# Performance work log

Hardware: AMD Instinct MI355X
Metric: run time of the kernel (lower is better)

## Reference

```python
import jax, jax.numpy as jnp
import numpy as np

T, C, H, W, D = 100, 2, 128, 128, 8192


def setup_inputs() -> dict:
    key = jax.random.key(0)
    k1, k2, k3, k4 = jax.random.split(key, 4)
    # event histogram: nonnegative intensities per (time, polarity, y, x)
    hist = jax.random.uniform(k1, (T, C, H, W), dtype=jnp.float32)
    # torchhd Random(vsa='MAP') tables are random bipolar {-1,+1} vectors
    time_w = jnp.sign(jax.random.normal(k2, (T, D), dtype=jnp.float32))
    pol_w = jnp.sign(jax.random.normal(k3, (C, D), dtype=jnp.float32))
    pos_w = jnp.sign(jax.random.normal(k4, (H * W, D), dtype=jnp.float32))
    return {"hist": hist, "time_w": time_w, "pol_w": pol_w, "pos_w": pos_w}


def reference(hist, time_w, pol_w, pos_w):
    # Original: for every nonzero pixel, bind (elementwise mul in MAP)
    # pos_hv * pol_hv * time_hv, scale by intensity, accumulate, then sign.
    # Equivalent fused form:
    #   out_d = sign( sum_{t,p,n} hist[t,p,n] * pos_w[n,d] * pol_w[p,d] * time_w[t,d] )
    t, c, h, w = hist.shape
    flat = hist.reshape(t, c, h * w)                      # [T, 2, H*W]
    # intensity-weighted sum of position HVs per (t, p): one GEMM over H*W
    acc = jnp.einsum('tpn,nd->tpd', flat, pos_w)          # [T, 2, D]
    # bind with polarity and time HVs, reduce over t and p
    gesture = jnp.einsum('tpd,pd,td->d', acc, pol_w, time_w)  # [D]
    return jnp.sign(gesture)
```

## Files before the change

### kernel.cpp

```cpp
#include <hip/hip_runtime.h>
#include <cstdint>
#include <cstddef>

#define MROWS 200
#define PM    224
#define KDIM  16384
#define DDIM  8192
#define KSL   16
#define KPER  (KDIM / KSL)
#define BK    32

typedef __bf16 bf16x8 __attribute__((ext_vector_type(8)));
typedef float  f32x4  __attribute__((ext_vector_type(4)));

static __device__ __forceinline__ unsigned short f2bf_rne(float f) {
    unsigned int u = __float_as_uint(f);
    unsigned int r = (u + 0x7FFFu + ((u >> 16) & 1u)) >> 16;
    return (unsigned short)r;
}
static __device__ __forceinline__ float bf2f(unsigned short s) {
    return __uint_as_float(((unsigned int)s) << 16);
}

static __device__ __forceinline__ void gld_lds16(const unsigned short* g,
                                                 unsigned short* l) {
    __builtin_amdgcn_global_load_lds(
        (const __attribute__((address_space(1))) unsigned int*)g,
        (__attribute__((address_space(3))) unsigned int*)l, 16, 0, 0);
}

__global__ __launch_bounds__(256) void zero_kernel(float* __restrict__ out) {
    out[blockIdx.x * 256 + threadIdx.x] = 0.f;
}

__global__ __launch_bounds__(256) void prep_kernel(const float* __restrict__ hist,
                                                   unsigned short* __restrict__ ahi,
                                                   unsigned short* __restrict__ alo) {
    const int g  = blockIdx.x * 256 + threadIdx.x;
    const int m  = g >> 11;
    const int gc = g & 2047;
    const int f  = (m >> 1) & 3;
    const int sgc = (gc & ~3) | ((gc & 3) ^ f);
    alignas(16) unsigned short hi[8], lo[8];
    if (m < MROWS) {
        const float* src = hist + (size_t)m * KDIM + sgc * 8;
        float4 a = *(const float4*)(src);
        float4 b = *(const float4*)(src + 4);
        const float v[8] = {a.x, a.y, a.z, a.w, b.x, b.y, b.z, b.w};
#pragma unroll
        for (int i = 0; i < 8; ++i) {
            unsigned short h = f2bf_rne(v[i]);
            hi[i] = h;
            lo[i] = f2bf_rne(v[i] - bf2f(h));
        }
    } else {
#pragma unroll
        for (int i = 0; i < 8; ++i) { hi[i] = 0; lo[i] = 0; }
    }
    *(uint4*)(ahi + (size_t)g * 8) = *(const uint4*)hi;
    *(uint4*)(alo + (size_t)g * 8) = *(const uint4*)lo;
}

__global__ __launch_bounds__(256, 2)
void gemm_kernel(const unsigned short* __restrict__ ahi,
                 const unsigned short* __restrict__ alo,
                 const float* __restrict__ pos,
                 const float* __restrict__ time_w,
                 const float* __restrict__ pol_w,
                 float* __restrict__ out) {
    __shared__ alignas(16) unsigned short As0[PM * BK];
    __shared__ alignas(16) unsigned short As1[PM * BK];
    __shared__ alignas(16) unsigned short Bs[128][40];
    __shared__ float sPart[128];

    const int t     = threadIdx.x;
    const int ks    = blockIdx.x;
    const int n0    = blockIdx.y * 128;
    const int kbase = ks * KPER;

    const int lane = t & 63;
    const int wv   = t >> 6;
    const int wm   = (wv & 1) * 112;
    const int wn   = (wv >> 1) * 64;
    const int l15  = lane & 15;
    const int q8   = (lane >> 4) * 8;
    const int qg   = (lane >> 4) ^ ((l15 >> 1) & 3);

    if (t < 128) sPart[t] = 0.f;

    const int lr = lane >> 2, lg = lane & 3;
    const unsigned short* gA[7];
    unsigned short* lA[7];
#pragma unroll
    for (int i = 0; i < 7; ++i) {
        const int cc = wv * 7 + i;
        const int pl = (cc >= 14) ? 1 : 0;
        const int ch = cc - pl * 14;
        gA[i] = (pl ? alo : ahi) + (size_t)(ch * 16 + lr) * KDIM + kbase + lg * 8;
        lA[i] = (pl ? As1 : As0) + ch * 512;
    }

    const int bk2 = (t & 15) * 2;
    const int bnb = (t >> 4) * 8;
    const float* gB0 = pos + ((size_t)kbase + bk2) * DDIM + n0 + bnb;
    const float* gB1 = gB0 + DDIM;

    f32x4 acc[7][4];
#pragma unroll
    for (int s = 0; s < 7; ++s)
#pragma unroll
        for (int j = 0; j < 4; ++j) acc[s][j] = (f32x4){0.f, 0.f, 0.f, 0.f};

    for (int kk = 0; kk < KPER; kk += BK) {
        const float* b0 = gB0 + (size_t)kk * DDIM;
        const float* b1 = gB1 + (size_t)kk * DDIM;
        float4 x0 = *(const float4*)(b0);
        float4 x1 = *(const float4*)(b0 + 4);
        float4 y0 = *(const float4*)(b1);
        float4 y1 = *(const float4*)(b1 + 4);

        __syncthreads();

#pragma unroll
        for (int i = 0; i < 7; ++i) gld_lds16(gA[i] + kk, lA[i]);

        {
            const float xv[8] = {x0.x, x0.y, x0.z, x0.w, x1.x, x1.y, x1.z, x1.w};
            const float yv[8] = {y0.x, y0.y, y0.z, y0.w, y1.x, y1.y, y1.z, y1.w};
#pragma unroll
            for (int j = 0; j < 8; ++j) {
                unsigned int w = (__float_as_uint(xv[j]) >> 16) |
                                 (__float_as_uint(yv[j]) & 0xFFFF0000u);
                *(unsigned int*)&Bs[bnb + j][bk2] = w;
            }
        }

        __syncthreads();

        uint4 fb[4];
#pragma unroll
        for (int j = 0; j < 4; ++j)
            fb[j] = *(const uint4*)&Bs[wn + j * 16 + l15][q8];

#pragma unroll
        for (int s = 0; s < 7; ++s) {
            const int mr = wm + s * 16 + l15;
            const uint4 fa0 = *(const uint4*)&As0[mr * 32 + qg * 8];
            const uint4 fa1 = *(const uint4*)&As1[mr * 32 + qg * 8];
#pragma unroll
            for (int j = 0; j < 4; ++j) {
                acc[s][j] = __builtin_amdgcn_mfma_f32_16x16x32_bf16(
                    __builtin_bit_cast(bf16x8, fa0),
                    __builtin_bit_cast(bf16x8, fb[j]), acc[s][j], 0, 0, 0);
                acc[s][j] = __builtin_amdgcn_mfma_f32_16x16x32_bf16(
                    __builtin_bit_cast(bf16x8, fa1),
                    __builtin_bit_cast(bf16x8, fb[j]), acc[s][j], 0, 0, 0);
            }
        }
    }

    const int qrow = (lane >> 4) * 4;
#pragma unroll
    for (int j = 0; j < 4; ++j) {
        const int col = wn + j * 16 + l15;
        const int d   = n0 + col;
        const float p0 = pol_w[d];
        const float p1 = pol_w[DDIM + d];
        float part = 0.f;
#pragma unroll
        for (int s = 0; s < 7; ++s)
#pragma unroll
            for (int r = 0; r < 4; ++r) {
                const int m = wm + s * 16 + qrow + r;
                if (m < MROWS) {
                    const float w = time_w[(size_t)(m >> 1) * DDIM + d] *
                                    ((m & 1) ? p1 : p0);
                    part += w * acc[s][j][r];
                }
            }
        atomicAdd(&sPart[col], part);
    }
    __syncthreads();
    if (t < 128) atomicAdd(out + n0 + t, sPart[t]);
}

__global__ __launch_bounds__(256) void sign_kernel(float* __restrict__ out) {
    int d = blockIdx.x * 256 + threadIdx.x;
    float s = out[d];
    out[d] = (s > 0.f) ? 1.f : ((s < 0.f) ? -1.f : 0.f);
}

extern "C" void kernel_launch(void* const* d_in, const int* in_sizes, int n_in,
                              void* d_out, int out_size, void* d_ws, size_t ws_size,
                              hipStream_t stream) {
    const float* hist   = (const float*)d_in[0];
    const float* time_w = (const float*)d_in[1];
    const float* pol_w  = (const float*)d_in[2];
    const float* pos_w  = (const float*)d_in[3];
    float* out = (float*)d_out;

    unsigned short* ahi = (unsigned short*)d_ws;
    unsigned short* alo = ahi + (size_t)PM * KDIM;
    (void)in_sizes; (void)n_in; (void)out_size; (void)ws_size;

    zero_kernel<<<DDIM / 256, 256, 0, stream>>>(out);
    prep_kernel<<<(PM * (KDIM / 8)) / 256, 256, 0, stream>>>(hist, ahi, alo);
    gemm_kernel<<<dim3(KSL, DDIM / 128), 256, 0, stream>>>(ahi, alo, pos_w,
                                                           time_w, pol_w, out);
    sign_kernel<<<DDIM / 256, 256, 0, stream>>>(out);
}
```

Measured before the change: 752.1 us.

## Software-pipeline GEMM with double-buffered A tiles and B register prefetch

Restructures the K loop of the GEMM so that A tiles are double-buffered in LDS and B rows are prefetched two steps ahead into registers. Explicit waitcnt, s_barrier and sched_barrier calls order the memory ops, and setprio raises wave priority during the MFMA section. The goal is to overlap global loads with MFMA work instead of stalling on each tile. In exchange it uses more LDS, which may limit occupancy, and more registers. Wrap-around indexing issues redundant loads at the end of the loop, and the hand-tuned vmcnt count makes correctness depend on load ordering.

```diff
diff --git a/kernel.cpp b/kernel.cpp
--- a/kernel.cpp
+++ b/kernel.cpp
@@ -9,6 +9,7 @@
 #define KSL   16
 #define KPER  (KDIM / KSL)
 #define BK    32
+#define NSTEP (KPER / BK)
 
 typedef __bf16 bf16x8 __attribute__((ext_vector_type(8)));
 typedef float  f32x4  __attribute__((ext_vector_type(4)));
@@ -68,8 +69,7 @@
                  const float* __restrict__ time_w,
                  const float* __restrict__ pol_w,
                  float* __restrict__ out) {
-    __shared__ alignas(16) unsigned short As0[PM * BK];
-    __shared__ alignas(16) unsigned short As1[PM * BK];
+    __shared__ alignas(16) unsigned short As[2][2][PM * BK];
     __shared__ alignas(16) unsigned short Bs[128][40];
     __shared__ float sPart[128];
 
@@ -90,14 +90,15 @@
 
     const int lr = lane >> 2, lg = lane & 3;
     const unsigned short* gA[7];
-    unsigned short* lA[7];
+    unsigned short* lA[2][7];
 #pragma unroll
     for (int i = 0; i < 7; ++i) {
         const int cc = wv * 7 + i;
         const int pl = (cc >= 14) ? 1 : 0;
         const int ch = cc - pl * 14;
         gA[i] = (pl ? alo : ahi) + (size_t)(ch * 16 + lr) * KDIM + kbase + lg * 8;
-        lA[i] = (pl ? As1 : As0) + ch * 512;
+        lA[0][i] = &As[0][pl][ch * 512];
+        lA[1][i] = &As[1][pl][ch * 512];
     }
 
     const int bk2 = (t & 15) * 2;
@@ -111,51 +112,88 @@
 #pragma unroll
         for (int j = 0; j < 4; ++j) acc[s][j] = (f32x4){0.f, 0.f, 0.f, 0.f};
 
-    for (int kk = 0; kk < KPER; kk += BK) {
-        const float* b0 = gB0 + (size_t)kk * DDIM;
-        const float* b1 = gB1 + (size_t)kk * DDIM;
-        float4 x0 = *(const float4*)(b0);
-        float4 x1 = *(const float4*)(b0 + 4);
-        float4 y0 = *(const float4*)(b1);
-        float4 y1 = *(const float4*)(b1 + 4);
-
-        __syncthreads();
-
-#pragma unroll
-        for (int i = 0; i < 7; ++i) gld_lds16(gA[i] + kk, lA[i]);
-
-        {
-            const float xv[8] = {x0.x, x0.y, x0.z, x0.w, x1.x, x1.y, x1.z, x1.w};
-            const float yv[8] = {y0.x, y0.y, y0.z, y0.w, y1.x, y1.y, y1.z, y1.w};
-#pragma unroll
-            for (int j = 0; j < 8; ++j) {
-                unsigned int w = (__float_as_uint(xv[j]) >> 16) |
-                                 (__float_as_uint(yv[j]) & 0xFFFF0000u);
-                *(unsigned int*)&Bs[bnb + j][bk2] = w;
-            }
-        }
-
-        __syncthreads();
-
-        uint4 fb[4];
-#pragma unroll
-        for (int j = 0; j < 4; ++j)
-            fb[j] = *(const uint4*)&Bs[wn + j * 16 + l15][q8];
-
-#pragma unroll
-        for (int s = 0; s < 7; ++s) {
-            const int mr = wm + s * 16 + l15;
-            const uint4 fa0 = *(const uint4*)&As0[mr * 32 + qg * 8];
-            const uint4 fa1 = *(const uint4*)&As1[mr * 32 + qg * 8];
-#pragma unroll
-            for (int j = 0; j < 4; ++j) {
-                acc[s][j] = __builtin_amdgcn_mfma_f32_16x16x32_bf16(
-                    __builtin_bit_cast(bf16x8, fa0),
-                    __builtin_bit_cast(bf16x8, fb[j]), acc[s][j], 0, 0, 0);
-                acc[s][j] = __builtin_amdgcn_mfma_f32_16x16x32_bf16(
-                    __builtin_bit_cast(bf16x8, fa1),
-                    __builtin_bit_cast(bf16x8, fb[j]), acc[s][j], 0, 0, 0);
-            }
+    float4 br[2][4];
+
+    br[0][0] = *(const float4*)(gB0);
+    br[0][1] = *(const float4*)(gB0 + 4);
+    br[0][2] = *(const float4*)(gB1);
+    br[0][3] = *(const float4*)(gB1 + 4);
+    __builtin_amdgcn_sched_barrier(0);
+#pragma unroll
+    for (int i = 0; i < 7; ++i) gld_lds16(gA[i], lA[0][i]);
+    __builtin_amdgcn_sched_barrier(0);
+    {
+        const size_t r1 = (size_t)BK * DDIM;
+        br[1][0] = *(const float4*)(gB0 + r1);
+        br[1][1] = *(const float4*)(gB0 + r1 + 4);
+        br[1][2] = *(const float4*)(gB1 + r1);
+        br[1][3] = *(const float4*)(gB1 + r1 + 4);
+    }
+    __builtin_amdgcn_sched_barrier(0);
+
+    for (int kp = 0; kp < NSTEP; kp += 2) {
+#pragma unroll
+        for (int u = 0; u < 2; ++u) {
+            const int kk = kp + u;
+
+            {
+                const float xv[8] = {br[u][0].x, br[u][0].y, br[u][0].z, br[u][0].w,
+                                     br[u][1].x, br[u][1].y, br[u][1].z, br[u][1].w};
+                const float yv[8] = {br[u][2].x, br[u][2].y, br[u][2].z, br[u][2].w,
+                                     br[u][3].x, br[u][3].y, br[u][3].z, br[u][3].w};
+#pragma unroll
+                for (int j = 0; j < 8; ++j) {
+                    unsigned int w = (__float_as_uint(xv[j]) >> 16) |
+                                     (__float_as_uint(yv[j]) & 0xFFFF0000u);
+                    *(unsigned int*)&Bs[bnb + j][bk2] = w;
+                }
+            }
+            asm volatile("s_waitcnt vmcnt(4) lgkmcnt(0)" ::: "memory");
+            __builtin_amdgcn_s_barrier();
+            __builtin_amdgcn_sched_barrier(0);
+
+            {
+                const int koff = ((kk + 1) & (NSTEP - 1)) * BK;
+#pragma unroll
+                for (int i = 0; i < 7; ++i)
+                    gld_lds16(gA[i] + koff, lA[u ^ 1][i]);
+            }
+            __builtin_amdgcn_sched_barrier(0);
+
+            uint4 fb[4];
+#pragma unroll
+            for (int j = 0; j < 4; ++j)
+                fb[j] = *(const uint4*)&Bs[wn + j * 16 + l15][q8];
+
+            __builtin_amdgcn_s_setprio(1);
+#pragma unroll
+            for (int s = 0; s < 7; ++s) {
+                const int mo = (wm + s * 16 + l15) * 32 + qg * 8;
+                const uint4 fa0 = *(const uint4*)&As[u][0][mo];
+                const uint4 fa1 = *(const uint4*)&As[u][1][mo];
+#pragma unroll
+                for (int j = 0; j < 4; ++j) {
+                    acc[s][j] = __builtin_amdgcn_mfma_f32_16x16x32_bf16(
+                        __builtin_bit_cast(bf16x8, fa0),
+                        __builtin_bit_cast(bf16x8, fb[j]), acc[s][j], 0, 0, 0);
+                    acc[s][j] = __builtin_amdgcn_mfma_f32_16x16x32_bf16(
+                        __builtin_bit_cast(bf16x8, fa1),
+                        __builtin_bit_cast(bf16x8, fb[j]), acc[s][j], 0, 0, 0);
+                }
+            }
+            __builtin_amdgcn_s_setprio(0);
+            __builtin_amdgcn_sched_barrier(0);
+            __builtin_amdgcn_s_barrier();
+            __builtin_amdgcn_sched_barrier(0);
+
+            {
+                const size_t roff = (size_t)((kk + 2) & (NSTEP - 1)) * BK * DDIM;
+                br[u][0] = *(const float4*)(gB0 + roff);
+                br[u][1] = *(const float4*)(gB0 + roff + 4);
+                br[u][2] = *(const float4*)(gB1 + roff);
+                br[u][3] = *(const float4*)(gB1 + roff + 4);
+            }
+            __builtin_amdgcn_sched_barrier(0);
         }
     }
 
```

After: 755.4 us. About the same (+0.4%).
